# Kernel tuning notes

Hardware: AMD Instinct MI355X
Metric: run time of the kernel (lower is better)

The kernel has to match this reference:

```python
import jax, jax.numpy as jnp
import numpy as np

NUM_VERTICES = 100_000
NUM_SPRINGS = 6_400_000
DIM = 3
EPS = 1e-6


def setup_inputs() -> dict:
    key = jax.random.key(0)
    k1, k2, k3, k4, k5 = jax.random.split(key, 5)
    x = jax.random.normal(k1, (NUM_VERTICES, DIM), dtype=jnp.float32)
    l0 = jax.random.uniform(k2, (NUM_SPRINGS,), dtype=jnp.float32)
    kk = jax.random.uniform(k3, (NUM_SPRINGS,), dtype=jnp.float32)
    i1 = jax.random.randint(k4, (NUM_SPRINGS,), 0, NUM_VERTICES, dtype=jnp.int64 if jax.config.read('jax_enable_x64') else jnp.int32)
    i2 = jax.random.randint(k5, (NUM_SPRINGS,), 0, NUM_VERTICES, dtype=i1.dtype)
    indices = jnp.stack([i1, i2], axis=1)  # [E, 2]
    return {"x": x, "l0": l0, "k": kk, "indices": indices}


def reference(x, l0, k, indices):
    # incidence.mm(x) with +1 at i1 and -1 at i2 per row == gather-based edge diff
    d = x[indices[:, 0]] - x[indices[:, 1]]        # [E, DIM]
    q = jnp.sum(d * d, axis=1)                     # [E]
    l = jnp.sqrt(q + EPS)                          # [E]
    dl = l - l0                                    # [E]
    e = 0.5 * jnp.sum(k * dl * dl)                 # scalar spring energy
    return e
```

## Files before the change

kernel.cpp:

```cpp
#include <hip/hip_runtime.h>
#include <math.h>

#define EPS 1e-6f

constexpr int BLOCK = 256;
constexpr int GRID  = 2048;

__global__ __launch_bounds__(BLOCK) void spring_energy_partial(
    const float* __restrict__ x,
    const float* __restrict__ l0,
    const float* __restrict__ k,
    const int*   __restrict__ idx,
    float* __restrict__ partials,
    int nsprings)
{
    const int tid      = blockIdx.x * BLOCK + threadIdx.x;
    const int nthreads = GRID * BLOCK;
    const int nquads   = nsprings >> 2;

    float acc = 0.f;
    for (int q = tid; q < nquads; q += nthreads) {
        const int s = q << 2;
        int4   ia  = *reinterpret_cast<const int4*>(idx + 2 * s);
        int4   ib  = *reinterpret_cast<const int4*>(idx + 2 * s + 4);
        float4 l0v = *reinterpret_cast<const float4*>(l0 + s);
        float4 kv  = *reinterpret_cast<const float4*>(k + s);

        const int   i1[4] = {ia.x, ia.z, ib.x, ib.z};
        const int   i2[4] = {ia.y, ia.w, ib.y, ib.w};
        const float lv[4] = {l0v.x, l0v.y, l0v.z, l0v.w};
        const float kvv[4]= {kv.x,  kv.y,  kv.z,  kv.w};

        #pragma unroll
        for (int j = 0; j < 4; ++j) {
            const float* p1 = x + 3 * i1[j];
            const float* p2 = x + 3 * i2[j];
            float dx = p1[0] - p2[0];
            float dy = p1[1] - p2[1];
            float dz = p1[2] - p2[2];
            float qd = dx*dx + dy*dy + dz*dz;
            float l  = sqrtf(qd + EPS);
            float dl = l - lv[j];
            acc = fmaf(kvv[j] * dl, dl, acc);
        }
    }

    if (blockIdx.x == 0) {
        for (int s = (nquads << 2) + threadIdx.x; s < nsprings; s += BLOCK) {
            int i1 = idx[2 * s], i2 = idx[2 * s + 1];
            const float* p1 = x + 3 * i1;
            const float* p2 = x + 3 * i2;
            float dx = p1[0] - p2[0];
            float dy = p1[1] - p2[1];
            float dz = p1[2] - p2[2];
            float l  = sqrtf(dx*dx + dy*dy + dz*dz + EPS);
            float dl = l - l0[s];
            acc = fmaf(k[s] * dl, dl, acc);
        }
    }

    #pragma unroll
    for (int off = 32; off > 0; off >>= 1)
        acc += __shfl_down(acc, off, 64);

    __shared__ float wsum[BLOCK / 64];
    const int lane = threadIdx.x & 63;
    const int wid  = threadIdx.x >> 6;
    if (lane == 0) wsum[wid] = acc;
    __syncthreads();
    if (threadIdx.x == 0)
        partials[blockIdx.x] = wsum[0] + wsum[1] + wsum[2] + wsum[3];
}

__global__ __launch_bounds__(BLOCK) void spring_energy_final(
    const float* __restrict__ partials,
    float* __restrict__ out)
{
    float acc = 0.f;
    for (int i = threadIdx.x; i < GRID; i += BLOCK)
        acc += partials[i];

    #pragma unroll
    for (int off = 32; off > 0; off >>= 1)
        acc += __shfl_down(acc, off, 64);

    __shared__ float wsum[BLOCK / 64];
    const int lane = threadIdx.x & 63;
    const int wid  = threadIdx.x >> 6;
    if (lane == 0) wsum[wid] = acc;
    __syncthreads();
    if (threadIdx.x == 0)
        out[0] = 0.5f * (wsum[0] + wsum[1] + wsum[2] + wsum[3]);
}

extern "C" void kernel_launch(void* const* d_in, const int* in_sizes, int n_in,
                              void* d_out, int out_size, void* d_ws, size_t ws_size,
                              hipStream_t stream) {
    const float* x   = (const float*)d_in[0];
    const float* l0  = (const float*)d_in[1];
    const float* k   = (const float*)d_in[2];
    const int*   idx = (const int*)  d_in[3];
    float* out       = (float*)d_out;
    float* partials  = (float*)d_ws;

    const int nsprings = in_sizes[1];

    spring_energy_partial<<<GRID, BLOCK, 0, stream>>>(x, l0, k, idx, partials, nsprings);
    spring_energy_final<<<1, BLOCK, 0, stream>>>(partials, out);
}
```

Measured before the change: 68.23 us.

## Gather vertices from padded fp16 copy and process eight springs per thread

Adds a pre-pass that converts vertex positions to half precision and pads them to 8-byte records, so each endpoint gather becomes a single 8-byte load instead of three scalar float loads. The main loop now handles eight springs per iteration and uses nontemporal loads for the streamed index, rest-length and stiffness arrays. The fp16 conversion lowers coordinate precision, which can shift the energy result beyond tolerance, and the extra kernel launch adds a small fixed cost.

```diff
diff --git a/kernel.cpp b/kernel.cpp
--- a/kernel.cpp
+++ b/kernel.cpp
@@ -6,8 +6,25 @@
 constexpr int BLOCK = 256;
 constexpr int GRID  = 2048;
 
+typedef int      vi4 __attribute__((ext_vector_type(4)));
+typedef float    vf4 __attribute__((ext_vector_type(4)));
+typedef _Float16 vh4 __attribute__((ext_vector_type(4)));
+
+__global__ __launch_bounds__(BLOCK) void pad_vertices(
+    const float* __restrict__ x,
+    vh4* __restrict__ xh,
+    int nverts)
+{
+    int v = blockIdx.x * BLOCK + threadIdx.x;
+    if (v < nverts) {
+        const float* p = x + 3 * v;
+        vh4 t = {(_Float16)p[0], (_Float16)p[1], (_Float16)p[2], (_Float16)0.f};
+        xh[v] = t;
+    }
+}
+
 __global__ __launch_bounds__(BLOCK) void spring_energy_partial(
-    const float* __restrict__ x,
+    const vh4*   __restrict__ xh,
     const float* __restrict__ l0,
     const float* __restrict__ k,
     const int*   __restrict__ idx,
@@ -16,43 +33,55 @@
 {
     const int tid      = blockIdx.x * BLOCK + threadIdx.x;
     const int nthreads = GRID * BLOCK;
-    const int nquads   = nsprings >> 2;
+    const int nocts    = nsprings >> 3;
 
     float acc = 0.f;
-    for (int q = tid; q < nquads; q += nthreads) {
-        const int s = q << 2;
-        int4   ia  = *reinterpret_cast<const int4*>(idx + 2 * s);
-        int4   ib  = *reinterpret_cast<const int4*>(idx + 2 * s + 4);
-        float4 l0v = *reinterpret_cast<const float4*>(l0 + s);
-        float4 kv  = *reinterpret_cast<const float4*>(k + s);
+    for (int o = tid; o < nocts; o += nthreads) {
+        const int s = o << 3;
+        const vi4* ip = reinterpret_cast<const vi4*>(idx + 2 * s);
+        vi4 i0 = __builtin_nontemporal_load(ip);
+        vi4 i1 = __builtin_nontemporal_load(ip + 1);
+        vi4 i2 = __builtin_nontemporal_load(ip + 2);
+        vi4 i3 = __builtin_nontemporal_load(ip + 3);
+        const vf4* lp = reinterpret_cast<const vf4*>(l0 + s);
+        vf4 la = __builtin_nontemporal_load(lp);
+        vf4 lb = __builtin_nontemporal_load(lp + 1);
+        const vf4* kp = reinterpret_cast<const vf4*>(k + s);
+        vf4 ka = __builtin_nontemporal_load(kp);
+        vf4 kb = __builtin_nontemporal_load(kp + 1);
 
-        const int   i1[4] = {ia.x, ia.z, ib.x, ib.z};
-        const int   i2[4] = {ia.y, ia.w, ib.y, ib.w};
-        const float lv[4] = {l0v.x, l0v.y, l0v.z, l0v.w};
-        const float kvv[4]= {kv.x,  kv.y,  kv.z,  kv.w};
+        vh4 A[8], B[8];
+        A[0] = xh[i0.x]; B[0] = xh[i0.y];
+        A[1] = xh[i0.z]; B[1] = xh[i0.w];
+        A[2] = xh[i1.x]; B[2] = xh[i1.y];
+        A[3] = xh[i1.z]; B[3] = xh[i1.w];
+        A[4] = xh[i2.x]; B[4] = xh[i2.y];
+        A[5] = xh[i2.z]; B[5] = xh[i2.w];
+        A[6] = xh[i3.x]; B[6] = xh[i3.y];
+        A[7] = xh[i3.z]; B[7] = xh[i3.w];
+
+        const float lv[8] = {la.x, la.y, la.z, la.w, lb.x, lb.y, lb.z, lb.w};
+        const float kv[8] = {ka.x, ka.y, ka.z, ka.w, kb.x, kb.y, kb.z, kb.w};
 
         #pragma unroll
-        for (int j = 0; j < 4; ++j) {
-            const float* p1 = x + 3 * i1[j];
-            const float* p2 = x + 3 * i2[j];
-            float dx = p1[0] - p2[0];
-            float dy = p1[1] - p2[1];
-            float dz = p1[2] - p2[2];
+        for (int j = 0; j < 8; ++j) {
+            float dx = (float)A[j].x - (float)B[j].x;
+            float dy = (float)A[j].y - (float)B[j].y;
+            float dz = (float)A[j].z - (float)B[j].z;
             float qd = dx*dx + dy*dy + dz*dz;
             float l  = sqrtf(qd + EPS);
             float dl = l - lv[j];
-            acc = fmaf(kvv[j] * dl, dl, acc);
+            acc = fmaf(kv[j] * dl, dl, acc);
         }
     }
 
     if (blockIdx.x == 0) {
-        for (int s = (nquads << 2) + threadIdx.x; s < nsprings; s += BLOCK) {
-            int i1 = idx[2 * s], i2 = idx[2 * s + 1];
-            const float* p1 = x + 3 * i1;
-            const float* p2 = x + 3 * i2;
-            float dx = p1[0] - p2[0];
-            float dy = p1[1] - p2[1];
-            float dz = p1[2] - p2[2];
+        for (int s = (nocts << 3) + threadIdx.x; s < nsprings; s += BLOCK) {
+            int a = idx[2 * s], b = idx[2 * s + 1];
+            vh4 pa = xh[a], pb = xh[b];
+            float dx = (float)pa.x - (float)pb.x;
+            float dy = (float)pa.y - (float)pb.y;
+            float dz = (float)pa.z - (float)pb.z;
             float l  = sqrtf(dx*dx + dy*dy + dz*dz + EPS);
             float dl = l - l0[s];
             acc = fmaf(k[s] * dl, dl, acc);
@@ -101,10 +130,14 @@
     const float* k   = (const float*)d_in[2];
     const int*   idx = (const int*)  d_in[3];
     float* out       = (float*)d_out;
-    float* partials  = (float*)d_ws;
 
+    const int nverts   = in_sizes[0] / 3;
     const int nsprings = in_sizes[1];
 
-    spring_energy_partial<<<GRID, BLOCK, 0, stream>>>(x, l0, k, idx, partials, nsprings);
+    vh4*   xh       = (vh4*)d_ws;
+    float* partials = (float*)((char*)d_ws + (size_t)nverts * sizeof(vh4));
+
+    pad_vertices<<<(nverts + BLOCK - 1) / BLOCK, BLOCK, 0, stream>>>(x, xh, nverts);
+    spring_energy_partial<<<GRID, BLOCK, 0, stream>>>(xh, l0, k, idx, partials, nsprings);
     spring_energy_final<<<1, BLOCK, 0, stream>>>(partials, out);
 }
```

Result: slower. 81.88 us (+20.0%).
